# Kernel optimization log

Measured on AMD Instinct MI355X. Metric: run time of the kernel, lower is better.

Reference implementation:

```python
import jax, jax.numpy as jnp
from jax import lax
import numpy as np


def setup_inputs() -> dict:
    key = jax.random.key(0)
    k1, k2, k3, k4 = jax.random.split(key, 4)
    H = W = 512
    N = 32
    return {
        "image": jax.random.normal(k1, (1, H, W), dtype=jnp.float32),
        "x": jax.random.normal(k2, (N, 1, H, W), dtype=jnp.float32),
        "KL_w": jax.random.normal(k3, (9, 1, 3, 3), dtype=jnp.float32) * 0.1,
        "KL_b": jax.random.normal(k4, (9,), dtype=jnp.float32) * 0.1,
    }


def reference(image, x, KL_w, KL_b):
    # Per-pixel 3x3 kernel generation: Conv2d(1 -> 9, 3x3, SAME) on the geometry image.
    # image: [1, H, W] (unbatched, 1 channel)
    K = lax.conv_general_dilated(
        image[None],              # [1, 1, H, W]
        KL_w,                     # [9, 1, 3, 3]
        window_strides=(1, 1),
        padding="SAME",
        dimension_numbers=("NCHW", "OIHW", "NCHW"),
    )[0] + KL_b[:, None, None]    # [9, H, W]
    H, W = K.shape[1], K.shape[2]
    Kp = jnp.transpose(K, (1, 2, 0))  # [H, W, 9]; channel c = 3*i + j (row-major 3x3)

    xs = x[:, 0]                               # [N, H, W]
    xp = jnp.pad(xs, ((0, 0), (1, 1), (1, 1)))  # zero pad, matches F.pad
    # Overlapping 3x3 patches as 9 shifted views, stacked row-major to match unfold order.
    patches = jnp.stack(
        [xp[:, i:i + H, j:j + W] for i in range(3) for j in range(3)], axis=-1
    )  # [N, H, W, 9]

    # Per-pixel FMA + reduce: y[n,h,w] = sum_k patches[n,h,w,k] * Kp[h,w,k]
    y = jnp.einsum("nhwk,hwk->nhw", patches, Kp)
    return y
```

## Files before the change

### kernel.cpp

```cpp
#include <hip/hip_runtime.h>

#define HH 512
#define WW 512
#define HWSZ (HH * WW)
#define NN 32

__global__ __launch_bounds__(256) void conv_k_kernel(const float* __restrict__ img,
                                                     const float* __restrict__ kw,
                                                     const float* __restrict__ kb,
                                                     float* __restrict__ K) {
    int idx = blockIdx.x * 256 + threadIdx.x;
    if (idx >= HWSZ) return;
    int h = idx >> 9;
    int w = idx & 511;

    float p[3][3];
#pragma unroll
    for (int i = 0; i < 3; ++i) {
#pragma unroll
        for (int j = 0; j < 3; ++j) {
            int hh = h + i - 1;
            int ww = w + j - 1;
            p[i][j] = (hh >= 0 && hh < HH && ww >= 0 && ww < WW) ? img[hh * WW + ww] : 0.0f;
        }
    }
#pragma unroll
    for (int c = 0; c < 9; ++c) {
        float acc = kb[c];
#pragma unroll
        for (int i = 0; i < 3; ++i)
#pragma unroll
            for (int j = 0; j < 3; ++j)
                acc = fmaf(p[i][j], kw[c * 9 + i * 3 + j], acc);
        K[c * HWSZ + idx] = acc;
    }
}

__global__ __launch_bounds__(256) void apply_kernel(const float* __restrict__ x,
                                                    const float* __restrict__ K,
                                                    float* __restrict__ y) {
    int t = blockIdx.x * 256 + threadIdx.x;
    int w4i = t & 127;
    int n   = (t >> 7) & 31;
    int h   = t >> 12;
    int w4  = w4i * 4;

    const float* xn = x + n * HWSZ;
    float a0 = 0.f, a1 = 0.f, a2 = 0.f, a3 = 0.f;

#pragma unroll
    for (int i = 0; i < 3; ++i) {
        int hh = h + i - 1;
        if (hh < 0 || hh >= HH) continue;
        const float* xr = xn + hh * WW;
        float xv[6];
#pragma unroll
        for (int j = 0; j < 6; ++j) {
            int ww = w4 - 1 + j;
            xv[j] = (ww >= 0 && ww < WW) ? xr[ww] : 0.0f;
        }
#pragma unroll
        for (int j = 0; j < 3; ++j) {
            int c = i * 3 + j;
            const float4 kv = *reinterpret_cast<const float4*>(&K[c * HWSZ + h * WW + w4]);
            a0 = fmaf(xv[j + 0], kv.x, a0);
            a1 = fmaf(xv[j + 1], kv.y, a1);
            a2 = fmaf(xv[j + 2], kv.z, a2);
            a3 = fmaf(xv[j + 3], kv.w, a3);
        }
    }
    float4 out = make_float4(a0, a1, a2, a3);
    *reinterpret_cast<float4*>(&y[n * HWSZ + h * WW + w4]) = out;
}

extern "C" void kernel_launch(void* const* d_in, const int* in_sizes, int n_in,
                              void* d_out, int out_size, void* d_ws, size_t ws_size,
                              hipStream_t stream) {
    const float* img = (const float*)d_in[0];
    const float* x   = (const float*)d_in[1];
    const float* kw  = (const float*)d_in[2];
    const float* kb  = (const float*)d_in[3];
    float* y = (float*)d_out;
    float* K = (float*)d_ws;

    conv_k_kernel<<<HWSZ / 256, 256, 0, stream>>>(img, kw, kb, K);

    int total_threads = NN * HH * (WW / 4);
    apply_kernel<<<total_threads / 256, 256, 0, stream>>>(x, K, y);
}
```

Baseline: 120.2 us.

## Fuse kernel generation into apply kernel with shared-memory row staging

Result: faster. 101.3 us (-15.8%).

```diff
diff --git a/kernel.cpp b/kernel.cpp
--- a/kernel.cpp
+++ b/kernel.cpp
@@ -3,74 +3,103 @@
 #define HH 512
 #define WW 512
 #define HWSZ (HH * WW)
-#define NN 32
+#define NPB 4
+#define RSTRIDE 520
 
-__global__ __launch_bounds__(256) void conv_k_kernel(const float* __restrict__ img,
+__global__ __launch_bounds__(128) void fused_smblock(const float* __restrict__ img,
+                                                     const float* __restrict__ x,
                                                      const float* __restrict__ kw,
                                                      const float* __restrict__ kb,
-                                                     float* __restrict__ K) {
-    int idx = blockIdx.x * 256 + threadIdx.x;
-    if (idx >= HWSZ) return;
-    int h = idx >> 9;
-    int w = idx & 511;
+                                                     float* __restrict__ y) {
+    __shared__ float rows[3][RSTRIDE];
+    const int tid = threadIdx.x;
+    const int h   = blockIdx.x;
+    const int n0  = blockIdx.y * NPB;
+    const int w4  = tid * 4;
 
-    float p[3][3];
+    if (tid < 3) { rows[tid][3] = 0.0f; rows[tid][516] = 0.0f; }
+
+    const bool vm1 = (h - 1) >= 0;
+    const bool vp1 = (h + 1) < HH;
+
+    {
+        float4 r0 = vm1 ? *reinterpret_cast<const float4*>(img + (h - 1) * WW + w4) : make_float4(0, 0, 0, 0);
+        float4 r1 =       *reinterpret_cast<const float4*>(img + h * WW + w4);
+        float4 r2 = vp1 ? *reinterpret_cast<const float4*>(img + (h + 1) * WW + w4) : make_float4(0, 0, 0, 0);
+        *reinterpret_cast<float4*>(&rows[0][w4 + 4]) = r0;
+        *reinterpret_cast<float4*>(&rows[1][w4 + 4]) = r1;
+        *reinterpret_cast<float4*>(&rows[2][w4 + 4]) = r2;
+    }
+    __syncthreads();
+
+    float iv[3][6];
 #pragma unroll
     for (int i = 0; i < 3; ++i) {
-#pragma unroll
-        for (int j = 0; j < 3; ++j) {
-            int hh = h + i - 1;
-            int ww = w + j - 1;
-            p[i][j] = (hh >= 0 && hh < HH && ww >= 0 && ww < WW) ? img[hh * WW + ww] : 0.0f;
-        }
+        float4 v = *reinterpret_cast<const float4*>(&rows[i][w4 + 4]);
+        iv[i][0] = rows[i][w4 + 3];
+        iv[i][1] = v.x; iv[i][2] = v.y; iv[i][3] = v.z; iv[i][4] = v.w;
+        iv[i][5] = rows[i][w4 + 8];
     }
+
+    float Kr[9][4];
 #pragma unroll
     for (int c = 0; c < 9; ++c) {
-        float acc = kb[c];
+        float b = kb[c];
+#pragma unroll
+        for (int p = 0; p < 4; ++p) Kr[c][p] = b;
 #pragma unroll
         for (int i = 0; i < 3; ++i)
 #pragma unroll
-            for (int j = 0; j < 3; ++j)
-                acc = fmaf(p[i][j], kw[c * 9 + i * 3 + j], acc);
-        K[c * HWSZ + idx] = acc;
+            for (int q = 0; q < 3; ++q) {
+                float wv = kw[c * 9 + i * 3 + q];
+#pragma unroll
+                for (int p = 0; p < 4; ++p)
+                    Kr[c][p] = fmaf(iv[i][p + q], wv, Kr[c][p]);
+            }
     }
-}
+    __syncthreads();
 
-__global__ __launch_bounds__(256) void apply_kernel(const float* __restrict__ x,
-                                                    const float* __restrict__ K,
-                                                    float* __restrict__ y) {
-    int t = blockIdx.x * 256 + threadIdx.x;
-    int w4i = t & 127;
-    int n   = (t >> 7) & 31;
-    int h   = t >> 12;
-    int w4  = w4i * 4;
+    float4 pr[3];
+    {
+        const float* base = x + (size_t)n0 * HWSZ;
+        pr[0] = vm1 ? *reinterpret_cast<const float4*>(base + (h - 1) * WW + w4) : make_float4(0, 0, 0, 0);
+        pr[1] =       *reinterpret_cast<const float4*>(base + h * WW + w4);
+        pr[2] = vp1 ? *reinterpret_cast<const float4*>(base + (h + 1) * WW + w4) : make_float4(0, 0, 0, 0);
+    }
 
-    const float* xn = x + n * HWSZ;
-    float a0 = 0.f, a1 = 0.f, a2 = 0.f, a3 = 0.f;
+    for (int nn = 0; nn < NPB; ++nn) {
+        *reinterpret_cast<float4*>(&rows[0][w4 + 4]) = pr[0];
+        *reinterpret_cast<float4*>(&rows[1][w4 + 4]) = pr[1];
+        *reinterpret_cast<float4*>(&rows[2][w4 + 4]) = pr[2];
+        __syncthreads();
 
+        if (nn + 1 < NPB) {
+            const float* base = x + (size_t)(n0 + nn + 1) * HWSZ;
+            pr[0] = vm1 ? *reinterpret_cast<const float4*>(base + (h - 1) * WW + w4) : make_float4(0, 0, 0, 0);
+            pr[1] =       *reinterpret_cast<const float4*>(base + h * WW + w4);
+            pr[2] = vp1 ? *reinterpret_cast<const float4*>(base + (h + 1) * WW + w4) : make_float4(0, 0, 0, 0);
+        }
+
+        float a[4] = {0, 0, 0, 0};
 #pragma unroll
-    for (int i = 0; i < 3; ++i) {
-        int hh = h + i - 1;
-        if (hh < 0 || hh >= HH) continue;
-        const float* xr = xn + hh * WW;
-        float xv[6];
+        for (int i = 0; i < 3; ++i) {
+            float xv[6];
+            float4 v = *reinterpret_cast<const float4*>(&rows[i][w4 + 4]);
+            xv[0] = rows[i][w4 + 3];
+            xv[1] = v.x; xv[2] = v.y; xv[3] = v.z; xv[4] = v.w;
+            xv[5] = rows[i][w4 + 8];
 #pragma unroll
-        for (int j = 0; j < 6; ++j) {
-            int ww = w4 - 1 + j;
-            xv[j] = (ww >= 0 && ww < WW) ? xr[ww] : 0.0f;
+            for (int j = 0; j < 3; ++j) {
+                const int c = i * 3 + j;
+#pragma unroll
+                for (int p = 0; p < 4; ++p)
+                    a[p] = fmaf(xv[p + j], Kr[c][p], a[p]);
+            }
         }
-#pragma unroll
-        for (int j = 0; j < 3; ++j) {
-            int c = i * 3 + j;
-            const float4 kv = *reinterpret_cast<const float4*>(&K[c * HWSZ + h * WW + w4]);
-            a0 = fmaf(xv[j + 0], kv.x, a0);
-            a1 = fmaf(xv[j + 1], kv.y, a1);
-            a2 = fmaf(xv[j + 2], kv.z, a2);
-            a3 = fmaf(xv[j + 3], kv.w, a3);
-        }
+        *reinterpret_cast<float4*>(&y[(size_t)(n0 + nn) * HWSZ + h * WW + w4]) =
+            make_float4(a[0], a[1], a[2], a[3]);
+        __syncthreads();
     }
-    float4 out = make_float4(a0, a1, a2, a3);
-    *reinterpret_cast<float4*>(&y[n * HWSZ + h * WW + w4]) = out;
 }
 
 extern "C" void kernel_launch(void* const* d_in, const int* in_sizes, int n_in,
@@ -81,10 +110,7 @@
     const float* kw  = (const float*)d_in[2];
     const float* kb  = (const float*)d_in[3];
     float* y = (float*)d_out;
-    float* K = (float*)d_ws;
 
-    conv_k_kernel<<<HWSZ / 256, 256, 0, stream>>>(img, kw, kb, K);
-
-    int total_threads = NN * HH * (WW / 4);
-    apply_kernel<<<total_threads / 256, 256, 0, stream>>>(x, K, y);
+    dim3 grid(HH, 32 / NPB);
+    fused_smblock<<<grid, 128, 0, stream>>>(img, x, kw, kb, y);
 }
```
